# Kernel optimization log

Measured on AMD Instinct MI355X. Metric: run time of the kernel, lower is better.

Reference implementation:

```python
import jax, jax.numpy as jnp
import numpy as np

N_NODES = 100000
N_EDGES = 1600000
IN_DIM, HID_DIM, OUT_DIM = 256, 128, 64


def gcn_conv(x, row, col, w, W, b, n):
    # PyG GCNConv (eval): add self-loops (weight 1), symmetric normalization,
    # linear transform, scatter-add aggregation at target nodes.
    row = jnp.concatenate([row, jnp.arange(n, dtype=row.dtype)])
    col = jnp.concatenate([col, jnp.arange(n, dtype=col.dtype)])
    w = jnp.concatenate([w, jnp.ones((n,), dtype=w.dtype)])
    deg = jax.ops.segment_sum(w, col, num_segments=n)  # [N]
    dinv = jnp.where(deg > 0, jax.lax.rsqrt(deg), 0.0)
    norm = dinv[row] * w * dinv[col]  # [E+N]
    h = x @ W  # [N, out]
    msg = norm[:, None] * h[row]  # gather: [E+N, out]
    out = jax.ops.segment_sum(msg, col, num_segments=n)  # scatter-add
    return out + b


def setup_inputs() -> dict:
    key = jax.random.key(0)
    k = jax.random.split(key, 8)
    x = jax.random.normal(k[0], (N_NODES, IN_DIM), dtype=jnp.float32)
    edge_index = jax.random.randint(k[1], (2, N_EDGES), 0, N_NODES, dtype=jnp.int64)
    edge_weight = jax.random.uniform(k[2], (N_EDGES,), dtype=jnp.float32)
    s1 = 1.0 / np.sqrt(IN_DIM)
    s2 = 1.0 / np.sqrt(HID_DIM)
    W1 = jax.random.uniform(k[3], (IN_DIM, HID_DIM), minval=-s1, maxval=s1, dtype=jnp.float32)
    b1 = jnp.zeros((HID_DIM,), dtype=jnp.float32)
    W2 = jax.random.uniform(k[4], (HID_DIM, OUT_DIM), minval=-s2, maxval=s2, dtype=jnp.float32)
    b2 = jnp.zeros((OUT_DIM,), dtype=jnp.float32)
    return {"x": x, "edge_index": edge_index, "edge_weight": edge_weight,
            "W1": W1, "b1": b1, "W2": W2, "b2": b2}


def reference(x, edge_index, edge_weight, W1, b1, W2, b2):
    row, col = edge_index[0], edge_index[1]
    n = x.shape[0]
    h = gcn_conv(x, row, col, edge_weight, W1, b1, n)
    h = jax.nn.relu(h)  # dropout is identity in eval mode
    out = gcn_conv(h, row, col, edge_weight, W2, b2, n)
    return out
```

## Files before the change

kernel.cpp:

```cpp
#include <hip/hip_runtime.h>
#include <hip/hip_fp16.h>

#define IN_DIM 256
#define HID_DIM 128
#define OUT_DIM 64

typedef short s8v __attribute__((ext_vector_type(8)));
typedef float f32x4 __attribute__((ext_vector_type(4)));


__device__ __forceinline__ unsigned short bf16_rne(float f) {
    unsigned int u = __float_as_uint(f);
    u += 0x7FFFu + ((u >> 16) & 1u);
    return (unsigned short)(u >> 16);
}
__device__ __forceinline__ float bfbits_to_f(unsigned short h) {
    return __uint_as_float(((unsigned int)h) << 16);
}
__device__ __forceinline__ void cvt_split4(float4 f, uint2& hv, uint2& lv) {
    unsigned short h0 = bf16_rne(f.x), h1 = bf16_rne(f.y);
    unsigned short h2 = bf16_rne(f.z), h3 = bf16_rne(f.w);
    unsigned short l0 = bf16_rne(f.x - bfbits_to_f(h0));
    unsigned short l1 = bf16_rne(f.y - bfbits_to_f(h1));
    unsigned short l2 = bf16_rne(f.z - bfbits_to_f(h2));
    unsigned short l3 = bf16_rne(f.w - bfbits_to_f(h3));
    hv.x = (unsigned int)h0 | ((unsigned int)h1 << 16);
    hv.y = (unsigned int)h2 | ((unsigned int)h3 << 16);
    lv.x = (unsigned int)l0 | ((unsigned int)l1 << 16);
    lv.y = (unsigned int)l2 | ((unsigned int)l3 << 16);
}

__device__ __forceinline__ void cvt_split8(float4 f0, float4 f1, s8v& hi, s8v& lo) {
    uint2 h0, l0, h1, l1;
    cvt_split4(f0, h0, l0);
    cvt_split4(f1, h1, l1);
    uint4 h = make_uint4(h0.x, h0.y, h1.x, h1.y);
    uint4 l = make_uint4(l0.x, l0.y, l1.x, l1.y);
    hi = *(s8v*)&h;
    lo = *(s8v*)&l;
}

__global__ __launch_bounds__(256) void wsplit_kernel(const float* __restrict__ W,
        unsigned short* __restrict__ wth, unsigned short* __restrict__ wtl,
        int K, int NCOL) {
    int idx = blockIdx.x * 256 + threadIdx.x;
    if (idx < K * NCOL) {
        int k = idx / NCOL, nn = idx % NCOL;
        float f = W[idx];
        unsigned short h = bf16_rne(f);
        unsigned short l = bf16_rne(f - bfbits_to_f(h));
        wth[nn * K + k] = h;
        wtl[nn * K + k] = l;
    }
}


#define FPSCALE 16777216.0f
#define FPMASK  ((1ULL << 40) - 1)

__global__ __launch_bounds__(256) void init_kernel(unsigned long long* packed, int n) {
    int i = blockIdx.x * 256 + threadIdx.x;
    if (i < n) packed[i] = (1ULL << 24);
}

__global__ __launch_bounds__(256) void deg_cnt_kernel(const int* __restrict__ col,
        const float* __restrict__ w, unsigned long long* packed,
        int* __restrict__ arr, int e) {
    int i = blockIdx.x * 256 + threadIdx.x;
    if (i < e) {
        unsigned long long v = (1ULL << 40) |
            (unsigned long long)(w[i] * FPSCALE + 0.5f);
        unsigned long long old = atomicAdd(&packed[col[i]], v);
        arr[i] = (int)(old >> 40);
    }
}

__global__ __launch_bounds__(256) void dinv_kernel(const unsigned long long* __restrict__ packed,
        float* __restrict__ dinv, int* __restrict__ cnt, int n) {
    int i = blockIdx.x * 256 + threadIdx.x;
    if (i < n) {
        unsigned long long p = packed[i];
        float d = (float)(p & FPMASK) * (1.0f / FPSCALE);
        dinv[i] = d > 0.0f ? rsqrtf(d) : 0.0f;
        cnt[i] = (int)(p >> 40);
    }
}


__global__ __launch_bounds__(256) void scan1_kernel(const int* __restrict__ cnt,
        int* __restrict__ bsum, int n) {
    int t = threadIdx.x;
    int base = blockIdx.x * 1024 + t * 4;
    int s = 0;
    if (base + 3 < n) {
        int4 v = *(const int4*)(cnt + base);
        s = v.x + v.y + v.z + v.w;
    } else {
        for (int i = 0; i < 4; i++) if (base + i < n) s += cnt[base + i];
    }
    __shared__ int sm[256];
    sm[t] = s;
    __syncthreads();
    for (int d = 1; d < 256; d <<= 1) {
        int v = (t >= d) ? sm[t - d] : 0;
        __syncthreads();
        sm[t] += v;
        __syncthreads();
    }
    if (t == 255) bsum[blockIdx.x] = sm[255];
}

__global__ __launch_bounds__(1024) void scan2_kernel(int* bsum, int* total_out, int nb) {
    __shared__ int sm[1024];
    int t = threadIdx.x;
    int v = (t < nb) ? bsum[t] : 0;
    sm[t] = v;
    __syncthreads();
    for (int d = 1; d < 1024; d <<= 1) {
        int u = (t >= d) ? sm[t - d] : 0;
        __syncthreads();
        sm[t] += u;
        __syncthreads();
    }
    int ex = (t == 0) ? 0 : sm[t - 1];
    if (t < nb) bsum[t] = ex;
    if (t == nb - 1) *total_out = sm[t];
}

__global__ __launch_bounds__(256) void scan3_kernel(const int* __restrict__ cnt,
        const int* __restrict__ bsum, int* __restrict__ offsets, int n) {
    int t = threadIdx.x;
    int base = blockIdx.x * 1024 + t * 4;
    int a[4] = {0, 0, 0, 0};
    if (base + 3 < n) {
        int4 v = *(const int4*)(cnt + base);
        a[0] = v.x; a[1] = v.y; a[2] = v.z; a[3] = v.w;
    } else {
        for (int i = 0; i < 4; i++) if (base + i < n) a[i] = cnt[base + i];
    }
    int s = a[0] + a[1] + a[2] + a[3];
    __shared__ int sm[256];
    sm[t] = s;
    __syncthreads();
    for (int d = 1; d < 256; d <<= 1) {
        int u = (t >= d) ? sm[t - d] : 0;
        __syncthreads();
        sm[t] += u;
        __syncthreads();
    }
    int pre = bsum[blockIdx.x] + ((t == 0) ? 0 : sm[t - 1]);
    int o0 = pre, o1 = o0 + a[0], o2 = o1 + a[1], o3 = o2 + a[2];
    if (base + 3 < n) {
        *(int4*)(offsets + base) = make_int4(o0, o1, o2, o3);
    } else {
        int o[4] = {o0, o1, o2, o3};
        for (int i = 0; i < 4; i++) if (base + i < n) offsets[base + i] = o[i];
    }
}


__global__ __launch_bounds__(256) void fill_csc_kernel(const int* __restrict__ row,
        const int* __restrict__ col, const float* __restrict__ w,
        const int* __restrict__ offsets, const int* __restrict__ arr,
        int2* __restrict__ csc, int e) {
    int i = blockIdx.x * 256 + threadIdx.x;
    if (i < e) {
        int c = col[i];
        int p = offsets[c] + arr[i];
        csc[p] = make_int2(row[i], __float_as_int(w[i]));
    }
}


template<int K, int NCOL>
__global__ __launch_bounds__(256) void gemm_mfma_kernel(
        const float* __restrict__ x, const unsigned short* __restrict__ wth,
        const unsigned short* __restrict__ wtl, const float* __restrict__ dinv,
        __half* __restrict__ out, int n) {
    constexpr int NT = NCOL / 16;
    constexpr int NCH = K / 32;
    constexpr int SEG_PER_WAVE = NT / 4;

    __shared__ unsigned short sBh[2][NCOL][32];
    __shared__ unsigned short sBl[2][NCOL][32];

    int t = threadIdx.x;
    int wave = t >> 6, lane = t & 63, quad = lane >> 4, r16 = lane & 15;
    long rowBase = (long)blockIdx.x * 128;

    f32x4 acc[2][NT];
#pragma unroll
    for (int mi = 0; mi < 2; mi++)
#pragma unroll
        for (int nt = 0; nt < NT; nt++) acc[mi][nt] = (f32x4)0.0f;

    long r0 = rowBase + wave * 32 + r16;       if (r0 > n - 1) r0 = n - 1;
    long r1 = rowBase + wave * 32 + 16 + r16;  if (r1 > n - 1) r1 = n - 1;
    const float* pa0 = x + r0 * K + quad * 8;
    const float* pa1 = x + r1 * K + quad * 8;

    int l4 = lane >> 2;
    int c8 = (lane & 3) * 8;

    auto stage = [&](int buf, int kc) {
#pragma unroll
        for (int j = 0; j < SEG_PER_WAVE; j++) {
            int s = wave + 4 * j;
            int r = s * 16 + l4;
            const unsigned short* gh = wth + (long)r * K + kc * 32 + c8;
            const unsigned short* gl = wtl + (long)r * K + kc * 32 + c8;
            __builtin_amdgcn_global_load_lds(
                (const __attribute__((address_space(1))) unsigned int*)gh,
                (__attribute__((address_space(3))) unsigned int*)&sBh[buf][s * 16][0],
                16, 0, 0);
            __builtin_amdgcn_global_load_lds(
                (const __attribute__((address_space(1))) unsigned int*)gl,
                (__attribute__((address_space(3))) unsigned int*)&sBl[buf][s * 16][0],
                16, 0, 0);
        }
    };

    stage(0, 0);
    float4 a0 = *(const float4*)(pa0);
    float4 a1 = *(const float4*)(pa0 + 4);
    float4 a2 = *(const float4*)(pa1);
    float4 a3 = *(const float4*)(pa1 + 4);
    __syncthreads();

    for (int kc = 0; kc < NCH; kc++) {
        int buf = kc & 1;
        if (kc + 1 < NCH) stage(buf ^ 1, kc + 1);

        s8v ah0, al0, ah1, al1;
        cvt_split8(a0, a1, ah0, al0);
        cvt_split8(a2, a3, ah1, al1);
        if (kc + 1 < NCH) {
            const float* q0 = pa0 + (kc + 1) * 32;
            const float* q1 = pa1 + (kc + 1) * 32;
            a0 = *(const float4*)(q0);
            a1 = *(const float4*)(q0 + 4);
            a2 = *(const float4*)(q1);
            a3 = *(const float4*)(q1 + 4);
        }
#pragma unroll
        for (int nt = 0; nt < NT; nt++) {
            s8v bh = *(const s8v*)&sBh[buf][nt * 16 + r16][quad * 8];
            s8v bl = *(const s8v*)&sBl[buf][nt * 16 + r16][quad * 8];
            acc[0][nt] = __builtin_amdgcn_mfma_f32_16x16x32_bf16(ah0, bh, acc[0][nt], 0, 0, 0);
            acc[0][nt] = __builtin_amdgcn_mfma_f32_16x16x32_bf16(al0, bh, acc[0][nt], 0, 0, 0);
            acc[0][nt] = __builtin_amdgcn_mfma_f32_16x16x32_bf16(ah0, bl, acc[0][nt], 0, 0, 0);
            acc[1][nt] = __builtin_amdgcn_mfma_f32_16x16x32_bf16(ah1, bh, acc[1][nt], 0, 0, 0);
            acc[1][nt] = __builtin_amdgcn_mfma_f32_16x16x32_bf16(al1, bh, acc[1][nt], 0, 0, 0);
            acc[1][nt] = __builtin_amdgcn_mfma_f32_16x16x32_bf16(ah1, bl, acc[1][nt], 0, 0, 0);
        }
        __syncthreads();
    }

#pragma unroll
    for (int mi = 0; mi < 2; mi++) {
        long gr0 = rowBase + wave * 32 + mi * 16 + quad * 4;
#pragma unroll
        for (int nt = 0; nt < NT; nt++) {
            f32x4 d = acc[mi][nt];
#pragma unroll
            for (int i = 0; i < 4; i++) {
                long gr = gr0 + i;
                if (gr < n) out[gr * NCOL + nt * 16 + r16] =
                    __float2half(d[i] * dinv[gr]);
            }
        }
    }
}


__device__ __forceinline__ void acc8(float* a, uint4 raw, float w) {
    __half2* hp = (__half2*)&raw;
    float2 f0 = __half22float2(hp[0]);
    float2 f1 = __half22float2(hp[1]);
    float2 f2 = __half22float2(hp[2]);
    float2 f3 = __half22float2(hp[3]);
    a[0] += w * f0.x; a[1] += w * f0.y; a[2] += w * f1.x; a[3] += w * f1.y;
    a[4] += w * f2.x; a[5] += w * f2.y; a[6] += w * f3.x; a[7] += w * f3.y;
}

__device__ __forceinline__ void acc4h(float* a, uint2 raw, float w) {
    __half2* hp = (__half2*)&raw;
    float2 f0 = __half22float2(hp[0]);
    float2 f1 = __half22float2(hp[1]);
    a[0] += w * f0.x; a[1] += w * f0.y; a[2] += w * f1.x; a[3] += w * f1.y;
}


__global__ __launch_bounds__(256) void agg1_kernel(const __half* __restrict__ h,
        const float* __restrict__ dinv, const int* __restrict__ offsets,
        const int2* __restrict__ csc, const float* __restrict__ b,
        float* __restrict__ out, int n) {
    int t = threadIdx.x;
    int lane = t & 63;
    int strm = lane >> 4;
    int li = lane & 15;
    int node = blockIdx.x * 4 + (t >> 6);
    if (node >= n) return;

    float a0[8] = {0,0,0,0,0,0,0,0};
    float a1[8] = {0,0,0,0,0,0,0,0};
    int s = offsets[node], e = offsets[node + 1];

    if (strm == 0) {
        uint4 raw = ((const uint4*)(h + (long)node * HID_DIM))[li];
        acc8(a0, raw, 1.0f);
    }

    int p = s + strm;
    for (; p + 4 < e; p += 8) {
        int2 e0 = csc[p], e1 = csc[p + 4];
        uint4 r0 = ((const uint4*)(h + (long)e0.x * HID_DIM))[li];
        uint4 r1 = ((const uint4*)(h + (long)e1.x * HID_DIM))[li];
        acc8(a0, r0, __int_as_float(e0.y));
        acc8(a1, r1, __int_as_float(e1.y));
    }
    if (p < e) {
        int2 e0 = csc[p];
        uint4 r0 = ((const uint4*)(h + (long)e0.x * HID_DIM))[li];
        acc8(a0, r0, __int_as_float(e0.y));
    }
#pragma unroll
    for (int j = 0; j < 8; j++) a0[j] += a1[j];
#pragma unroll
    for (int j = 0; j < 8; j++) a0[j] += __shfl_down(a0[j], 32);
#pragma unroll
    for (int j = 0; j < 8; j++) a0[j] += __shfl_down(a0[j], 16);
    if (strm == 0) {
        float di = dinv[node];
        float4 bv0 = ((const float4*)b)[li * 2];
        float4 bv1 = ((const float4*)b)[li * 2 + 1];
        float4 o0 = make_float4(fmaxf(di * a0[0] + bv0.x, 0.f), fmaxf(di * a0[1] + bv0.y, 0.f),
                                fmaxf(di * a0[2] + bv0.z, 0.f), fmaxf(di * a0[3] + bv0.w, 0.f));
        float4 o1 = make_float4(fmaxf(di * a0[4] + bv1.x, 0.f), fmaxf(di * a0[5] + bv1.y, 0.f),
                                fmaxf(di * a0[6] + bv1.z, 0.f), fmaxf(di * a0[7] + bv1.w, 0.f));
        float4* dst = (float4*)(out + (long)node * HID_DIM);
        dst[li * 2] = o0;
        dst[li * 2 + 1] = o1;
    }
}


__global__ __launch_bounds__(256) void agg2_kernel(const __half* __restrict__ h,
        const float* __restrict__ dinv, const int* __restrict__ offsets,
        const int2* __restrict__ csc, const float* __restrict__ b,
        float* __restrict__ out, int n) {
    int t = threadIdx.x;
    int lane = t & 63;
    int strm = lane >> 4;
    int li = lane & 15;
    int node = blockIdx.x * 4 + (t >> 6);
    if (node >= n) return;

    float a0[4] = {0,0,0,0};
    float a1[4] = {0,0,0,0};
    int s = offsets[node], e = offsets[node + 1];

    if (strm == 0) {
        uint2 raw = ((const uint2*)(h + (long)node * OUT_DIM))[li];
        acc4h(a0, raw, 1.0f);
    }

    int p = s + strm;
    for (; p + 4 < e; p += 8) {
        int2 e0 = csc[p], e1 = csc[p + 4];
        uint2 r0 = ((const uint2*)(h + (long)e0.x * OUT_DIM))[li];
        uint2 r1 = ((const uint2*)(h + (long)e1.x * OUT_DIM))[li];
        acc4h(a0, r0, __int_as_float(e0.y));
        acc4h(a1, r1, __int_as_float(e1.y));
    }
    if (p < e) {
        int2 e0 = csc[p];
        uint2 r0 = ((const uint2*)(h + (long)e0.x * OUT_DIM))[li];
        acc4h(a0, r0, __int_as_float(e0.y));
    }
#pragma unroll
    for (int j = 0; j < 4; j++) a0[j] += a1[j];
#pragma unroll
    for (int j = 0; j < 4; j++) a0[j] += __shfl_down(a0[j], 32);
#pragma unroll
    for (int j = 0; j < 4; j++) a0[j] += __shfl_down(a0[j], 16);
    if (strm == 0) {
        float di = dinv[node];
        float4 bv = ((const float4*)b)[li];
        ((float4*)(out + (long)node * OUT_DIM))[li] =
            make_float4(di * a0[0] + bv.x, di * a0[1] + bv.y,
                        di * a0[2] + bv.z, di * a0[3] + bv.w);
    }
}


extern "C" void kernel_launch(void* const* d_in, const int* in_sizes, int n_in,
                              void* d_out, int out_size, void* d_ws, size_t ws_size,
                              hipStream_t stream) {
    const float* x  = (const float*)d_in[0];
    const int*   ei = (const int*)d_in[1];
    const float* w  = (const float*)d_in[2];
    const float* W1 = (const float*)d_in[3];
    const float* b1 = (const float*)d_in[4];
    const float* W2 = (const float*)d_in[5];
    const float* b2 = (const float*)d_in[6];
    float* out = (float*)d_out;

    int N = in_sizes[0] / IN_DIM;
    int E = in_sizes[2];
    const int* row = ei;
    const int* col = ei + E;

    char* base = (char*)d_ws;
    size_t off = 0;
    auto alloc = [&](size_t bytes) -> void* {
        void* p = base + off;
        off += (bytes + 255) & ~(size_t)255;
        return p;
    };
    unsigned long long* packed = (unsigned long long*)alloc((size_t)N * 8);
    float* dinv     = (float*)alloc((size_t)N * 4);
    int*   cnt      = (int*)  alloc((size_t)N * 4);
    int*   offsets  = (int*)  alloc((size_t)(N + 1) * 4);
    int*   arr      = (int*)  alloc((size_t)E * 4);
    int*   bsum     = (int*)  alloc((size_t)1024 * 4);
    int2*  csc      = (int2*) alloc((size_t)E * 8);
    __half* h       = (__half*)alloc((size_t)N * HID_DIM * 2);
    float* hagg     = (float*)alloc((size_t)N * HID_DIM * 4);
    unsigned short* wt1h = (unsigned short*)alloc((size_t)IN_DIM * HID_DIM * 2);
    unsigned short* wt1l = (unsigned short*)alloc((size_t)IN_DIM * HID_DIM * 2);
    unsigned short* wt2h = (unsigned short*)alloc((size_t)HID_DIM * OUT_DIM * 2);
    unsigned short* wt2l = (unsigned short*)alloc((size_t)HID_DIM * OUT_DIM * 2);

    int gN = (N + 255) / 256;
    int gE = (E + 255) / 256;
    int gGemm = (N + 127) / 128;
    int gAgg = (N + 3) / 4;
    int nbScan = (N + 1023) / 1024;

    wsplit_kernel<<<(IN_DIM * HID_DIM + 255) / 256, 256, 0, stream>>>(
        W1, wt1h, wt1l, IN_DIM, HID_DIM);
    wsplit_kernel<<<(HID_DIM * OUT_DIM + 255) / 256, 256, 0, stream>>>(
        W2, wt2h, wt2l, HID_DIM, OUT_DIM);
    init_kernel<<<gN, 256, 0, stream>>>(packed, N);
    deg_cnt_kernel<<<gE, 256, 0, stream>>>(col, w, packed, arr, E);
    dinv_kernel<<<gN, 256, 0, stream>>>(packed, dinv, cnt, N);
    scan1_kernel<<<nbScan, 256, 0, stream>>>(cnt, bsum, N);
    scan2_kernel<<<1, 1024, 0, stream>>>(bsum, offsets + N, nbScan);
    scan3_kernel<<<nbScan, 256, 0, stream>>>(cnt, bsum, offsets, N);
    fill_csc_kernel<<<gE, 256, 0, stream>>>(row, col, w, offsets, arr, csc, E);
    gemm_mfma_kernel<IN_DIM, HID_DIM><<<gGemm, 256, 0, stream>>>(x, wt1h, wt1l, dinv, h, N);
    agg1_kernel<<<gAgg, 256, 0, stream>>>(h, dinv, offsets, csc, b1, hagg, N);
    gemm_mfma_kernel<HID_DIM, OUT_DIM><<<gGemm, 256, 0, stream>>>(hagg, wt2h, wt2l, dinv, h, N);
    agg2_kernel<<<gAgg, 256, 0, stream>>>(h, dinv, offsets, csc, b2, out, N);
}
```

Measured before the change: 480.8 us.

## Retile GEMM to 2 waves x 64 rows with swizzled LDS and packed bf16 split

The MFMA GEMM now uses 128-thread blocks. Each wave owns 64 rows (four 16-row M tiles), so every B fragment read from LDS is reused across four M tiles instead of two. The B tile staging applies an XOR swizzle to the LDS slot to reduce bank conflicts on reads. The fp32 to bf16 hi/lo split uses paired __float22bfloat162_rn conversions, and dinv is hoisted out of the store loop. The tradeoff is more accumulator and A-fragment registers per thread, half as many waves per block to hide latency, and twice as many B loads issued per wave.

```diff
diff --git a/kernel.cpp b/kernel.cpp
--- a/kernel.cpp
+++ b/kernel.cpp
@@ -1,5 +1,6 @@
 #include <hip/hip_runtime.h>
 #include <hip/hip_fp16.h>
+#include <hip/hip_bf16.h>
 
 #define IN_DIM 256
 #define HID_DIM 128
@@ -17,27 +18,23 @@
 __device__ __forceinline__ float bfbits_to_f(unsigned short h) {
     return __uint_as_float(((unsigned int)h) << 16);
 }
-__device__ __forceinline__ void cvt_split4(float4 f, uint2& hv, uint2& lv) {
-    unsigned short h0 = bf16_rne(f.x), h1 = bf16_rne(f.y);
-    unsigned short h2 = bf16_rne(f.z), h3 = bf16_rne(f.w);
-    unsigned short l0 = bf16_rne(f.x - bfbits_to_f(h0));
-    unsigned short l1 = bf16_rne(f.y - bfbits_to_f(h1));
-    unsigned short l2 = bf16_rne(f.z - bfbits_to_f(h2));
-    unsigned short l3 = bf16_rne(f.w - bfbits_to_f(h3));
-    hv.x = (unsigned int)h0 | ((unsigned int)h1 << 16);
-    hv.y = (unsigned int)h2 | ((unsigned int)h3 << 16);
-    lv.x = (unsigned int)l0 | ((unsigned int)l1 << 16);
-    lv.y = (unsigned int)l2 | ((unsigned int)l3 << 16);
-}
 
 __device__ __forceinline__ void cvt_split8(float4 f0, float4 f1, s8v& hi, s8v& lo) {
-    uint2 h0, l0, h1, l1;
-    cvt_split4(f0, h0, l0);
-    cvt_split4(f1, h1, l1);
-    uint4 h = make_uint4(h0.x, h0.y, h1.x, h1.y);
-    uint4 l = make_uint4(l0.x, l0.y, l1.x, l1.y);
-    hi = *(s8v*)&h;
-    lo = *(s8v*)&l;
+    float fv[8] = {f0.x, f0.y, f0.z, f0.w, f1.x, f1.y, f1.z, f1.w};
+    unsigned int hw[4], lw[4];
+#pragma unroll
+    for (int i = 0; i < 4; i++) {
+        __hip_bfloat162 hh = __float22bfloat162_rn(make_float2(fv[2*i], fv[2*i+1]));
+        unsigned int hb = *(unsigned int*)&hh;
+        float r0 = __uint_as_float(hb << 16);
+        float r1 = __uint_as_float(hb & 0xffff0000u);
+        __hip_bfloat162 ll = __float22bfloat162_rn(
+            make_float2(fv[2*i] - r0, fv[2*i+1] - r1));
+        hw[i] = hb;
+        lw[i] = *(unsigned int*)&ll;
+    }
+    hi = *(s8v*)hw;
+    lo = *(s8v*)lw;
 }
 
 __global__ __launch_bounds__(256) void wsplit_kernel(const float* __restrict__ W,
@@ -173,42 +170,45 @@
 
 
 template<int K, int NCOL>
-__global__ __launch_bounds__(256) void gemm_mfma_kernel(
+__global__ __launch_bounds__(128, 2) void gemm_mfma_kernel(
         const float* __restrict__ x, const unsigned short* __restrict__ wth,
         const unsigned short* __restrict__ wtl, const float* __restrict__ dinv,
         __half* __restrict__ out, int n) {
     constexpr int NT = NCOL / 16;
     constexpr int NCH = K / 32;
-    constexpr int SEG_PER_WAVE = NT / 4;
+    constexpr int NS = NCOL / 16;
 
     __shared__ unsigned short sBh[2][NCOL][32];
     __shared__ unsigned short sBl[2][NCOL][32];
 
     int t = threadIdx.x;
     int wave = t >> 6, lane = t & 63, quad = lane >> 4, r16 = lane & 15;
-    long rowBase = (long)blockIdx.x * 128;
-
-    f32x4 acc[2][NT];
-#pragma unroll
-    for (int mi = 0; mi < 2; mi++)
+    long rowBase = (long)blockIdx.x * 128 + wave * 64;
+
+    f32x4 acc[4][NT];
+#pragma unroll
+    for (int mi = 0; mi < 4; mi++)
 #pragma unroll
         for (int nt = 0; nt < NT; nt++) acc[mi][nt] = (f32x4)0.0f;
 
-    long r0 = rowBase + wave * 32 + r16;       if (r0 > n - 1) r0 = n - 1;
-    long r1 = rowBase + wave * 32 + 16 + r16;  if (r1 > n - 1) r1 = n - 1;
-    const float* pa0 = x + r0 * K + quad * 8;
-    const float* pa1 = x + r1 * K + quad * 8;
-
-    int l4 = lane >> 2;
-    int c8 = (lane & 3) * 8;
+    const float* pa[4];
+#pragma unroll
+    for (int mi = 0; mi < 4; mi++) {
+        long r = rowBase + mi * 16 + r16;
+        if (r > n - 1) r = n - 1;
+        pa[mi] = x + r * K + quad * 8;
+    }
+
+    int srcSlot = ((lane & 3) ^ ((lane >> 3) & 3)) * 8;
+    int lrow = lane >> 2;
 
     auto stage = [&](int buf, int kc) {
 #pragma unroll
-        for (int j = 0; j < SEG_PER_WAVE; j++) {
-            int s = wave + 4 * j;
-            int r = s * 16 + l4;
-            const unsigned short* gh = wth + (long)r * K + kc * 32 + c8;
-            const unsigned short* gl = wtl + (long)r * K + kc * 32 + c8;
+        for (int j = 0; j < NS / 2; j++) {
+            int s = wave + 2 * j;
+            int r = s * 16 + lrow;
+            const unsigned short* gh = wth + (long)r * K + kc * 32 + srcSlot;
+            const unsigned short* gl = wtl + (long)r * K + kc * 32 + srcSlot;
             __builtin_amdgcn_global_load_lds(
                 (const __attribute__((address_space(1))) unsigned int*)gh,
                 (__attribute__((address_space(3))) unsigned int*)&sBh[buf][s * 16][0],
@@ -221,44 +221,54 @@
     };
 
     stage(0, 0);
-    float4 a0 = *(const float4*)(pa0);
-    float4 a1 = *(const float4*)(pa0 + 4);
-    float4 a2 = *(const float4*)(pa1);
-    float4 a3 = *(const float4*)(pa1 + 4);
+    float4 a[8];
+#pragma unroll
+    for (int mi = 0; mi < 4; mi++) {
+        a[2 * mi]     = *(const float4*)(pa[mi]);
+        a[2 * mi + 1] = *(const float4*)(pa[mi] + 4);
+    }
     __syncthreads();
+
+    int rdSlot = (r16 >> 1) & 3;
 
     for (int kc = 0; kc < NCH; kc++) {
         int buf = kc & 1;
         if (kc + 1 < NCH) stage(buf ^ 1, kc + 1);
 
-        s8v ah0, al0, ah1, al1;
-        cvt_split8(a0, a1, ah0, al0);
-        cvt_split8(a2, a3, ah1, al1);
+        s8v ah[4], al[4];
+#pragma unroll
+        for (int mi = 0; mi < 4; mi++)
+            cvt_split8(a[2 * mi], a[2 * mi + 1], ah[mi], al[mi]);
         if (kc + 1 < NCH) {
-            const float* q0 = pa0 + (kc + 1) * 32;
-            const float* q1 = pa1 + (kc + 1) * 32;
-            a0 = *(const float4*)(q0);
-            a1 = *(const float4*)(q0 + 4);
-            a2 = *(const float4*)(q1);
-            a3 = *(const float4*)(q1 + 4);
+#pragma unroll
+            for (int mi = 0; mi < 4; mi++) {
+                const float* q = pa[mi] + (kc + 1) * 32;
+                a[2 * mi]     = *(const float4*)(q);
+                a[2 * mi + 1] = *(const float4*)(q + 4);
+            }
         }
 #pragma unroll
         for (int nt = 0; nt < NT; nt++) {
-            s8v bh = *(const s8v*)&sBh[buf][nt * 16 + r16][quad * 8];
-            s8v bl = *(const s8v*)&sBl[buf][nt * 16 + r16][quad * 8];
-            acc[0][nt] = __builtin_amdgcn_mfma_f32_16x16x32_bf16(ah0, bh, acc[0][nt], 0, 0, 0);
-            acc[0][nt] = __builtin_amdgcn_mfma_f32_16x16x32_bf16(al0, bh, acc[0][nt], 0, 0, 0);
-            acc[0][nt] = __builtin_amdgcn_mfma_f32_16x16x32_bf16(ah0, bl, acc[0][nt], 0, 0, 0);
-            acc[1][nt] = __builtin_amdgcn_mfma_f32_16x16x32_bf16(ah1, bh, acc[1][nt], 0, 0, 0);
-            acc[1][nt] = __builtin_amdgcn_mfma_f32_16x16x32_bf16(al1, bh, acc[1][nt], 0, 0, 0);
-            acc[1][nt] = __builtin_amdgcn_mfma_f32_16x16x32_bf16(ah1, bl, acc[1][nt], 0, 0, 0);
+            int sl = (quad ^ rdSlot) * 8;
+            s8v bh = *(const s8v*)&sBh[buf][nt * 16 + r16][sl];
+            s8v bl = *(const s8v*)&sBl[buf][nt * 16 + r16][sl];
+#pragma unroll
+            for (int mi = 0; mi < 4; mi++) {
+                acc[mi][nt] = __builtin_amdgcn_mfma_f32_16x16x32_bf16(ah[mi], bh, acc[mi][nt], 0, 0, 0);
+                acc[mi][nt] = __builtin_amdgcn_mfma_f32_16x16x32_bf16(al[mi], bh, acc[mi][nt], 0, 0, 0);
+                acc[mi][nt] = __builtin_amdgcn_mfma_f32_16x16x32_bf16(ah[mi], bl, acc[mi][nt], 0, 0, 0);
+            }
         }
         __syncthreads();
     }
 
 #pragma unroll
-    for (int mi = 0; mi < 2; mi++) {
-        long gr0 = rowBase + wave * 32 + mi * 16 + quad * 4;
+    for (int mi = 0; mi < 4; mi++) {
+        long gr0 = rowBase + mi * 16 + quad * 4;
+        float dv[4];
+#pragma unroll
+        for (int i = 0; i < 4; i++)
+            dv[i] = (gr0 + i < n) ? dinv[gr0 + i] : 0.0f;
 #pragma unroll
         for (int nt = 0; nt < NT; nt++) {
             f32x4 d = acc[mi][nt];
@@ -266,7 +276,7 @@
             for (int i = 0; i < 4; i++) {
                 long gr = gr0 + i;
                 if (gr < n) out[gr * NCOL + nt * 16 + r16] =
-                    __float2half(d[i] * dinv[gr]);
+                    __float2half(d[i] * dv[i]);
             }
         }
     }
@@ -449,8 +459,8 @@
     scan2_kernel<<<1, 1024, 0, stream>>>(bsum, offsets + N, nbScan);
     scan3_kernel<<<nbScan, 256, 0, stream>>>(cnt, bsum, offsets, N);
     fill_csc_kernel<<<gE, 256, 0, stream>>>(row, col, w, offsets, arr, csc, E);
-    gemm_mfma_kernel<IN_DIM, HID_DIM><<<gGemm, 256, 0, stream>>>(x, wt1h, wt1l, dinv, h, N);
+    gemm_mfma_kernel<IN_DIM, HID_DIM><<<gGemm, 128, 0, stream>>>(x, wt1h, wt1l, dinv, h, N);
     agg1_kernel<<<gAgg, 256, 0, stream>>>(h, dinv, offsets, csc, b1, hagg, N);
-    gemm_mfma_kernel<HID_DIM, OUT_DIM><<<gGemm, 256, 0, stream>>>(hagg, wt2h, wt2l, dinv, h, N);
+    gemm_mfma_kernel<HID_DIM, OUT_DIM><<<gGemm, 128, 0, stream>>>(hagg, wt2h, wt2l, dinv, h, N);
     agg2_kernel<<<gAgg, 256, 0, stream>>>(h, dinv, offsets, csc, b2, out, N);
 }
```

After: 470.6 us. 1.02x faster.
